# Optimization experiments

Measured on AMD Instinct MI355X. Metric: run time of the kernel, lower is better.

## Reference

```python
import jax, jax.numpy as jnp
import numpy as np

N_FFT = 1024
HOP = 256
WIN_LENGTH = 1024
B = 16
T = 480000


def setup_inputs() -> dict:
    key = jax.random.key(0)
    k1, k2 = jax.random.split(key)
    x = jax.random.normal(k1, (B, T), dtype=jnp.float32)
    window = jax.random.uniform(k2, (WIN_LENGTH,), dtype=jnp.float32)
    return {"x": x, "window": window}


def _dft_kernels(window):
    # pad window to n_fft if needed (here win_length == n_fft)
    if WIN_LENGTH < N_FFT:
        pl = (N_FFT - WIN_LENGTH) // 2
        window = jnp.pad(window, (pl, N_FFT - WIN_LENGTH - pl))
    n_freq = N_FFT // 2 + 1
    k = jnp.arange(n_freq, dtype=jnp.float32)[:, None]   # [F,1]
    n = jnp.arange(N_FFT, dtype=jnp.float32)[None, :]    # [1,N]
    basis = (2.0 * np.pi / N_FFT) * k * n                # [F,N]
    cos_k = jnp.cos(basis) * window[None, :]
    sin_k = -jnp.sin(basis) * window[None, :]
    return cos_k, sin_k


def reference(x, window):
    pad = N_FFT // 2
    xp = jnp.pad(x, ((0, 0), (pad, pad)), mode="reflect")  # center=True, reflect
    n_frames = (xp.shape[1] - N_FFT) // HOP + 1
    # frame extraction: [n_frames, n_fft] gather indices (strided windows)
    idx = jnp.arange(n_frames)[:, None] * HOP + jnp.arange(N_FFT)[None, :]
    frames = xp[:, idx]                                   # [B, n_frames, n_fft]
    cos_k, sin_k = _dft_kernels(window)                   # [F, n_fft]
    real = jnp.einsum("btn,fn->btf", frames, cos_k)        # [B, n_frames, F]
    imag = jnp.einsum("btn,fn->btf", frames, sin_k)
    return jnp.stack([real, imag], axis=-1)               # [B, n_frames, F, 2]
```

## Files before the change

### kernel.cpp

```cpp
#include <hip/hip_runtime.h>

#define BATCH     16
#define T_LEN     480000
#define PAD       512
#define TPAD      481024
#define HOP       256
#define NFRAMES   1876
#define NOUTROW   1026
#define KTOT      1024
#define BCOLS     1152
#define XPSTRIDE  493568

#define BM        256
#define BN        256
#define BK        32
#define NTILES    32
#define TILEA     16384
#define BUFBYTES  32768
#define NBUF      3
#define LDSBYTES  (NBUF * BUFBYTES)

typedef __attribute__((ext_vector_type(8))) short short8;
typedef __attribute__((ext_vector_type(4))) float floatx4;

#define GPTR(p) (const __attribute__((address_space(1))) void*)(p)
#define LPTR(p) (__attribute__((address_space(3))) void*)(p)

__device__ __forceinline__ unsigned short f2bf(float f) {
  union { float f; unsigned int u; } v; v.f = f;
  unsigned int u = v.u;
  return (unsigned short)((u + 0x7FFFu + ((u >> 16) & 1u)) >> 16);
}

__global__ __launch_bounds__(256) void build_xp(const float* __restrict__ x,
                                                unsigned short* __restrict__ xp) {
  const int i0 = (blockIdx.x * 256 + threadIdx.x) * 8;
  const int b  = blockIdx.y;
  const float* xb = x + (size_t)b * T_LEN;
  const int j0 = i0 - PAD;
  union { short8 v; unsigned short u[8]; } o;
  if (j0 >= 0 && j0 + 8 <= T_LEN) {
    const float4 lo = *(const float4*)(xb + j0);
    const float4 hi = *(const float4*)(xb + j0 + 4);
    o.u[0] = f2bf(lo.x); o.u[1] = f2bf(lo.y); o.u[2] = f2bf(lo.z); o.u[3] = f2bf(lo.w);
    o.u[4] = f2bf(hi.x); o.u[5] = f2bf(hi.y); o.u[6] = f2bf(hi.z); o.u[7] = f2bf(hi.w);
  } else {
#pragma unroll
    for (int e = 0; e < 8; ++e) {
      const int i = i0 + e;
      unsigned short v = 0;
      if (i < TPAD) {
        int j = i - PAD;
        if (j < 0) j = -j;
        if (j >= T_LEN) j = 2 * T_LEN - 2 - j;
        v = f2bf(xb[j]);
      }
      o.u[e] = v;
    }
  }
  *(short8*)(xp + (size_t)b * XPSTRIDE + i0) = o.v;
}

__global__ __launch_bounds__(256) void build_bmat(const float* __restrict__ win,
                                                  unsigned short* __restrict__ bm) {
  const int id = blockIdx.x * 256 + threadIdx.x;
  const int j  = id >> 7;
  const int k0 = (id & 127) * 8;
  union { short8 v; unsigned short u[8]; } o;
  if (j < NOUTROW) {
    const int f = j >> 1;
    const float4 w0 = *(const float4*)(win + k0);
    const float4 w1 = *(const float4*)(win + k0 + 4);
    const float wv[8] = {w0.x, w0.y, w0.z, w0.w, w1.x, w1.y, w1.z, w1.w};
#pragma unroll
    for (int e = 0; e < 8; ++e) {
      const int r = (f * (k0 + e)) & (KTOT - 1);
      const float ang = (float)r * 6.1359231515e-3f;
      const float c = __cosf(ang), s = __sinf(ang);
      o.u[e] = f2bf(((j & 1) ? -s : c) * wv[e]);
    }
  } else {
#pragma unroll
    for (int e = 0; e < 8; ++e) o.u[e] = 0;
  }
  *(short8*)(bm + (size_t)j * KTOT + k0) = o.v;
}

__global__ __launch_bounds__(512, 2) void stft_gemm(const unsigned short* __restrict__ xp,
                                                    const unsigned short* __restrict__ bmat,
                                                    float* __restrict__ out) {
  extern __shared__ char smemc[];

  const int tid  = threadIdx.x;
  const int lane = tid & 63;
  const int wv   = tid >> 6;
  const int wm   = wv >> 2;
  const int wn   = wv & 3;
  const int L    = lane & 15;
  const int quad = lane >> 4;
  const int b    = blockIdx.x >> 3;
  const int t0   = (blockIdx.x & 7) * BM;
  const int j0   = blockIdx.y * BN;

  const int srow = tid & 255;
  const int skq  = tid >> 8;
  const unsigned short* asrc =
      xp + (size_t)b * XPSTRIDE + (size_t)(t0 + srow) * HOP + skq * 8;
  int jc = j0 + srow;
  if (jc > BCOLS - 1) jc = BCOLS - 1;
  const unsigned short* bsrc = bmat + (size_t)jc * KTOT + skq * 8;

#define STAGE_A(KT, S)                                                         \
  __builtin_amdgcn_global_load_lds(GPTR(asrc + (KT) * BK),                     \
      LPTR(smemc + (S) * BUFBYTES + tid * 16), 16, 0, 0);                      \
  __builtin_amdgcn_global_load_lds(GPTR(asrc + (KT) * BK + 16),                \
      LPTR(smemc + (S) * BUFBYTES + 8192 + tid * 16), 16, 0, 0)
#define STAGE_B(KT, S)                                                         \
  __builtin_amdgcn_global_load_lds(GPTR(bsrc + (KT) * BK),                     \
      LPTR(smemc + (S) * BUFBYTES + TILEA + tid * 16), 16, 0, 0);              \
  __builtin_amdgcn_global_load_lds(GPTR(bsrc + (KT) * BK + 16),                \
      LPTR(smemc + (S) * BUFBYTES + TILEA + 8192 + tid * 16), 16, 0, 0)

  const int aoff = (quad * 256 + wm * 128 + L) * 16;
  const int boff = TILEA + (quad * 256 + wn * 64 + L) * 16;

  floatx4 acc[8][4] = {};
  short8 af[4], bf[4];

#define PHASE0(C, S, KT2, DOSTAGE)                                             \
  {                                                                            \
    const char* tb_ = smemc + (C) * BUFBYTES;                                  \
    _Pragma("unroll") for (int m = 0; m < 4; ++m)                              \
      af[m] = *(const short8*)(tb_ + aoff + m * 256);                          \
    _Pragma("unroll") for (int n = 0; n < 4; ++n)                              \
      bf[n] = *(const short8*)(tb_ + boff + n * 256);                          \
    if (DOSTAGE) { STAGE_A(KT2, S); }                                          \
    __builtin_amdgcn_s_barrier();                                              \
    __builtin_amdgcn_s_setprio(1);                                             \
    _Pragma("unroll") for (int m = 0; m < 4; ++m)                              \
      _Pragma("unroll") for (int n = 0; n < 4; ++n)                            \
        acc[m][n] = __builtin_amdgcn_mfma_f32_16x16x32_bf16(                   \
            af[m], bf[n], acc[m][n], 0, 0, 0);                                 \
    __builtin_amdgcn_s_setprio(0);                                             \
    __builtin_amdgcn_s_barrier();                                              \
  }
#define PHASE1(C, S, KT2, DOSTAGE, VM)                                         \
  {                                                                            \
    const char* tb_ = smemc + (C) * BUFBYTES;                                  \
    _Pragma("unroll") for (int m = 0; m < 4; ++m)                              \
      af[m] = *(const short8*)(tb_ + aoff + (m + 4) * 256);                    \
    if (DOSTAGE) { STAGE_B(KT2, S); }                                          \
    __builtin_amdgcn_s_barrier();                                              \
    __builtin_amdgcn_s_setprio(1);                                             \
    _Pragma("unroll") for (int m = 0; m < 4; ++m)                              \
      _Pragma("unroll") for (int n = 0; n < 4; ++n)                            \
        acc[m + 4][n] = __builtin_amdgcn_mfma_f32_16x16x32_bf16(               \
            af[m], bf[n], acc[m + 4][n], 0, 0, 0);                             \
    __builtin_amdgcn_s_setprio(0);                                             \
    asm volatile("s_waitcnt vmcnt(" #VM ")" ::: "memory");                     \
    __builtin_amdgcn_s_barrier();                                              \
  }

  STAGE_A(0, 0); STAGE_B(0, 0);
  STAGE_A(1, 1); STAGE_B(1, 1);
  asm volatile("s_waitcnt vmcnt(4)" ::: "memory");
  __builtin_amdgcn_s_barrier();

  for (int g = 0; g < 10; ++g) {
    const int k = 3 * g;
    PHASE0(0, 2, k + 2, 1);  PHASE1(0, 2, k + 2, 1, 4);
    PHASE0(1, 0, k + 3, 1);  PHASE1(1, 0, k + 3, 1, 4);
    PHASE0(2, 1, k + 4, 1);  PHASE1(2, 1, k + 4, 1, 4);
  }
  PHASE0(0, 0, 0, 0);  PHASE1(0, 0, 0, 0, 0);
  PHASE0(1, 0, 0, 0);  PHASE1(1, 0, 0, 0, 0);

#pragma unroll
  for (int mi = 0; mi < 8; ++mi) {
    const int tb = t0 + wm * 128 + mi * 16 + quad * 4;
#pragma unroll
    for (int ni = 0; ni < 4; ++ni) {
      const int gj = j0 + wn * 64 + ni * 16 + L;
      if (gj < NOUTROW) {
#pragma unroll
        for (int i = 0; i < 4; ++i) {
          const int t = tb + i;
          if (t < NFRAMES)
            out[(size_t)(b * NFRAMES + t) * NOUTROW + gj] = acc[mi][ni][i];
        }
      }
    }
  }
}

extern "C" void kernel_launch(void* const* d_in, const int* in_sizes, int n_in,
                              void* d_out, int out_size, void* d_ws, size_t ws_size,
                              hipStream_t stream) {
  const float* x   = (const float*)d_in[0];
  const float* win = (const float*)d_in[1];
  float* out = (float*)d_out;

  unsigned short* xp   = (unsigned short*)d_ws;
  unsigned short* bmat = xp + (size_t)BATCH * XPSTRIDE;

  (void)hipFuncSetAttribute((const void*)stft_gemm,
                            hipFuncAttributeMaxDynamicSharedMemorySize,
                            LDSBYTES);

  build_xp  <<<dim3(XPSTRIDE / 2048, BATCH), 256, 0, stream>>>(x, xp);
  build_bmat<<<dim3(BCOLS * (KTOT / 8) / 256), 256, 0, stream>>>(win, bmat);
  stft_gemm <<<dim3(BATCH * 8, 5), 512, LDSBYTES, stream>>>(xp, bmat, out);
}
```

Before: 259.7 us.

## Split Nyquist bin into separate kernel and shrink GEMM N-tile to avoid padding

The GEMM now covers only the first 1024 output columns (512 frequencies times real and imaginary) with 128-wide N tiles, 256 threads and static double-buffered LDS, replacing the 3-buffer phase-interleaved pipeline. The Nyquist bin (f=512) is computed by a new reduction kernel that writes the last two columns. This removes the padded 1152-column work, of which 126 columns were wasted, but adds an extra launch and uses a simpler, possibly less latency-hiding pipeline. Grid becomes 128x8 blocks.

```diff
diff --git a/kernel.cpp b/kernel.cpp
--- a/kernel.cpp
+++ b/kernel.cpp
@@ -8,17 +8,16 @@
 #define NFRAMES   1876
 #define NOUTROW   1026
 #define KTOT      1024
-#define BCOLS     1152
+#define BCOLS     1024
 #define XPSTRIDE  493568
 
 #define BM        256
-#define BN        256
+#define BN        128
 #define BK        32
 #define NTILES    32
-#define TILEA     16384
-#define BUFBYTES  32768
-#define NBUF      3
-#define LDSBYTES  (NBUF * BUFBYTES)
+#define ABUF      16384
+#define BBUF      8192
+#define BUFB      (ABUF + BBUF)
 
 typedef __attribute__((ext_vector_type(8))) short short8;
 typedef __attribute__((ext_vector_type(4))) float floatx4;
@@ -66,128 +65,128 @@
   const int id = blockIdx.x * 256 + threadIdx.x;
   const int j  = id >> 7;
   const int k0 = (id & 127) * 8;
+  const int f  = j >> 1;
+  const float4 w0 = *(const float4*)(win + k0);
+  const float4 w1 = *(const float4*)(win + k0 + 4);
+  const float wv[8] = {w0.x, w0.y, w0.z, w0.w, w1.x, w1.y, w1.z, w1.w};
   union { short8 v; unsigned short u[8]; } o;
-  if (j < NOUTROW) {
-    const int f = j >> 1;
-    const float4 w0 = *(const float4*)(win + k0);
-    const float4 w1 = *(const float4*)(win + k0 + 4);
-    const float wv[8] = {w0.x, w0.y, w0.z, w0.w, w1.x, w1.y, w1.z, w1.w};
-#pragma unroll
-    for (int e = 0; e < 8; ++e) {
-      const int r = (f * (k0 + e)) & (KTOT - 1);
-      const float ang = (float)r * 6.1359231515e-3f;
-      const float c = __cosf(ang), s = __sinf(ang);
-      o.u[e] = f2bf(((j & 1) ? -s : c) * wv[e]);
-    }
-  } else {
-#pragma unroll
-    for (int e = 0; e < 8; ++e) o.u[e] = 0;
+#pragma unroll
+  for (int e = 0; e < 8; ++e) {
+    const int r = (f * (k0 + e)) & (KTOT - 1);
+    const float ang = (float)r * 6.1359231515e-3f;
+    const float c = __cosf(ang), s = __sinf(ang);
+    o.u[e] = f2bf(((j & 1) ? -s : c) * wv[e]);
   }
   *(short8*)(bm + (size_t)j * KTOT + k0) = o.v;
 }
 
-__global__ __launch_bounds__(512, 2) void stft_gemm(const unsigned short* __restrict__ xp,
+__global__ __launch_bounds__(256) void f512_col(const unsigned short* __restrict__ xp,
+                                                const float* __restrict__ win,
+                                                float* __restrict__ out) {
+  const int t = blockIdx.x * 4 + (threadIdx.x >> 6);
+  const int b = blockIdx.y;
+  const int l = threadIdx.x & 63;
+  const unsigned short* xw = xp + (size_t)b * XPSTRIDE + (size_t)t * HOP;
+  float s = 0.f;
+#pragma unroll
+  for (int j = 0; j < 16; ++j) {
+    const int k = j * 64 + l;
+    union { unsigned int u; float f; } cv;
+    cv.u = (unsigned int)xw[k] << 16;
+    s += win[k] * cv.f;
+  }
+  if (l & 1) s = -s;
+#pragma unroll
+  for (int off = 32; off > 0; off >>= 1) s += __shfl_down(s, off, 64);
+  if (l == 0)
+    *(float2*)(out + (size_t)(b * NFRAMES + t) * NOUTROW + 1024) = make_float2(s, 0.f);
+}
+
+__global__ __launch_bounds__(256, 2) void stft_gemm(const unsigned short* __restrict__ xp,
                                                     const unsigned short* __restrict__ bmat,
                                                     float* __restrict__ out) {
-  extern __shared__ char smemc[];
+  __shared__ char smem[2 * BUFB];
 
   const int tid  = threadIdx.x;
   const int lane = tid & 63;
   const int wv   = tid >> 6;
-  const int wm   = wv >> 2;
-  const int wn   = wv & 3;
+  const int wm   = wv >> 1;
+  const int wn   = wv & 1;
   const int L    = lane & 15;
   const int quad = lane >> 4;
   const int b    = blockIdx.x >> 3;
   const int t0   = (blockIdx.x & 7) * BM;
   const int j0   = blockIdx.y * BN;
 
-  const int srow = tid & 255;
-  const int skq  = tid >> 8;
-  const unsigned short* asrc =
-      xp + (size_t)b * XPSTRIDE + (size_t)(t0 + srow) * HOP + skq * 8;
-  int jc = j0 + srow;
-  if (jc > BCOLS - 1) jc = BCOLS - 1;
-  const unsigned short* bsrc = bmat + (size_t)jc * KTOT + skq * 8;
-
-#define STAGE_A(KT, S)                                                         \
-  __builtin_amdgcn_global_load_lds(GPTR(asrc + (KT) * BK),                     \
-      LPTR(smemc + (S) * BUFBYTES + tid * 16), 16, 0, 0);                      \
-  __builtin_amdgcn_global_load_lds(GPTR(asrc + (KT) * BK + 16),                \
-      LPTR(smemc + (S) * BUFBYTES + 8192 + tid * 16), 16, 0, 0)
-#define STAGE_B(KT, S)                                                         \
-  __builtin_amdgcn_global_load_lds(GPTR(bsrc + (KT) * BK),                     \
-      LPTR(smemc + (S) * BUFBYTES + TILEA + tid * 16), 16, 0, 0);              \
-  __builtin_amdgcn_global_load_lds(GPTR(bsrc + (KT) * BK + 16),                \
-      LPTR(smemc + (S) * BUFBYTES + TILEA + 8192 + tid * 16), 16, 0, 0)
-
-  const int aoff = (quad * 256 + wm * 128 + L) * 16;
-  const int boff = TILEA + (quad * 256 + wn * 64 + L) * 16;
+  const unsigned short* asrc = xp + (size_t)b * XPSTRIDE + (size_t)(t0 + tid) * HOP;
+  const int col = tid & 127;
+  const int kqb = tid >> 7;
+  const unsigned short* bsrc0 = bmat + (size_t)(j0 + col) * KTOT + kqb * 8;
+  const unsigned short* bsrc1 = bmat + (size_t)(j0 + col) * KTOT + (2 + kqb) * 8;
+
+#define STAGE(T1, NB)                                                          \
+  {                                                                            \
+    const int ko_ = (T1) * BK;                                                 \
+    _Pragma("unroll") for (int p = 0; p < 4; ++p)                              \
+      __builtin_amdgcn_global_load_lds(GPTR(asrc + ko_ + p * 8),               \
+          LPTR((NB) + (p * 256 + tid) * 16), 16, 0, 0);                        \
+    __builtin_amdgcn_global_load_lds(GPTR(bsrc0 + ko_),                        \
+        LPTR((NB) + ABUF + tid * 16), 16, 0, 0);                               \
+    __builtin_amdgcn_global_load_lds(GPTR(bsrc1 + ko_),                        \
+        LPTR((NB) + ABUF + (256 + tid) * 16), 16, 0, 0);                       \
+  }
+
+  const int aof = (quad * 256 + wm * 128 + L) * 16;
+  const int bof = ABUF + (quad * 128 + wn * 64 + L) * 16;
 
   floatx4 acc[8][4] = {};
-  short8 af[4], bf[4];
-
-#define PHASE0(C, S, KT2, DOSTAGE)                                             \
-  {                                                                            \
-    const char* tb_ = smemc + (C) * BUFBYTES;                                  \
-    _Pragma("unroll") for (int m = 0; m < 4; ++m)                              \
-      af[m] = *(const short8*)(tb_ + aoff + m * 256);                          \
-    _Pragma("unroll") for (int n = 0; n < 4; ++n)                              \
-      bf[n] = *(const short8*)(tb_ + boff + n * 256);                          \
-    if (DOSTAGE) { STAGE_A(KT2, S); }                                          \
-    __builtin_amdgcn_s_barrier();                                              \
-    __builtin_amdgcn_s_setprio(1);                                             \
-    _Pragma("unroll") for (int m = 0; m < 4; ++m)                              \
-      _Pragma("unroll") for (int n = 0; n < 4; ++n)                            \
-        acc[m][n] = __builtin_amdgcn_mfma_f32_16x16x32_bf16(                   \
-            af[m], bf[n], acc[m][n], 0, 0, 0);                                 \
-    __builtin_amdgcn_s_setprio(0);                                             \
-    __builtin_amdgcn_s_barrier();                                              \
-  }
-#define PHASE1(C, S, KT2, DOSTAGE, VM)                                         \
-  {                                                                            \
-    const char* tb_ = smemc + (C) * BUFBYTES;                                  \
-    _Pragma("unroll") for (int m = 0; m < 4; ++m)                              \
-      af[m] = *(const short8*)(tb_ + aoff + (m + 4) * 256);                    \
-    if (DOSTAGE) { STAGE_B(KT2, S); }                                          \
-    __builtin_amdgcn_s_barrier();                                              \
-    __builtin_amdgcn_s_setprio(1);                                             \
-    _Pragma("unroll") for (int m = 0; m < 4; ++m)                              \
-      _Pragma("unroll") for (int n = 0; n < 4; ++n)                            \
-        acc[m + 4][n] = __builtin_amdgcn_mfma_f32_16x16x32_bf16(               \
-            af[m], bf[n], acc[m + 4][n], 0, 0, 0);                             \
-    __builtin_amdgcn_s_setprio(0);                                             \
-    asm volatile("s_waitcnt vmcnt(" #VM ")" ::: "memory");                     \
-    __builtin_amdgcn_s_barrier();                                              \
-  }
-
-  STAGE_A(0, 0); STAGE_B(0, 0);
-  STAGE_A(1, 1); STAGE_B(1, 1);
-  asm volatile("s_waitcnt vmcnt(4)" ::: "memory");
-  __builtin_amdgcn_s_barrier();
-
-  for (int g = 0; g < 10; ++g) {
-    const int k = 3 * g;
-    PHASE0(0, 2, k + 2, 1);  PHASE1(0, 2, k + 2, 1, 4);
-    PHASE0(1, 0, k + 3, 1);  PHASE1(1, 0, k + 3, 1, 4);
-    PHASE0(2, 1, k + 4, 1);  PHASE1(2, 1, k + 4, 1, 4);
-  }
-  PHASE0(0, 0, 0, 0);  PHASE1(0, 0, 0, 0, 0);
-  PHASE0(1, 0, 0, 0);  PHASE1(1, 0, 0, 0, 0);
-
-#pragma unroll
-  for (int mi = 0; mi < 8; ++mi) {
-    const int tb = t0 + wm * 128 + mi * 16 + quad * 4;
-#pragma unroll
-    for (int ni = 0; ni < 4; ++ni) {
-      const int gj = j0 + wn * 64 + ni * 16 + L;
-      if (gj < NOUTROW) {
-#pragma unroll
-        for (int i = 0; i < 4; ++i) {
-          const int t = tb + i;
-          if (t < NFRAMES)
-            out[(size_t)(b * NFRAMES + t) * NOUTROW + gj] = acc[mi][ni][i];
-        }
+
+  STAGE(0, (char*)smem);
+  __syncthreads();
+
+  for (int T = 0; T < NTILES; ++T) {
+    const char* cb = (const char*)smem + (T & 1) * BUFB;
+    char* nb = (char*)smem + ((T + 1) & 1) * BUFB;
+    if (T + 1 < NTILES) STAGE(T + 1, nb);
+
+    short8 af[4], bf[4];
+#pragma unroll
+    for (int n = 0; n < 4; ++n) bf[n] = *(const short8*)(cb + bof + n * 256);
+#pragma unroll
+    for (int m = 0; m < 4; ++m) af[m] = *(const short8*)(cb + aof + m * 256);
+    __builtin_amdgcn_s_setprio(1);
+#pragma unroll
+    for (int m = 0; m < 4; ++m)
+#pragma unroll
+      for (int n = 0; n < 4; ++n)
+        acc[m][n] = __builtin_amdgcn_mfma_f32_16x16x32_bf16(
+            af[m], bf[n], acc[m][n], 0, 0, 0);
+    __builtin_amdgcn_s_setprio(0);
+#pragma unroll
+    for (int m = 0; m < 4; ++m) af[m] = *(const short8*)(cb + aof + (m + 4) * 256);
+    __builtin_amdgcn_s_setprio(1);
+#pragma unroll
+    for (int m = 0; m < 4; ++m)
+#pragma unroll
+      for (int n = 0; n < 4; ++n)
+        acc[m + 4][n] = __builtin_amdgcn_mfma_f32_16x16x32_bf16(
+            af[m], bf[n], acc[m + 4][n], 0, 0, 0);
+    __builtin_amdgcn_s_setprio(0);
+
+    __syncthreads();
+  }
+
+#pragma unroll
+  for (int mf = 0; mf < 8; ++mf) {
+    const int tb = t0 + wm * 128 + mf * 16 + quad * 4;
+#pragma unroll
+    for (int n = 0; n < 4; ++n) {
+      const int gj = j0 + wn * 64 + n * 16 + L;
+#pragma unroll
+      for (int i = 0; i < 4; ++i) {
+        const int t = tb + i;
+        if (t < NFRAMES)
+          out[(size_t)(b * NFRAMES + t) * NOUTROW + gj] = acc[mf][n][i];
       }
     }
   }
@@ -203,11 +202,8 @@
   unsigned short* xp   = (unsigned short*)d_ws;
   unsigned short* bmat = xp + (size_t)BATCH * XPSTRIDE;
 
-  (void)hipFuncSetAttribute((const void*)stft_gemm,
-                            hipFuncAttributeMaxDynamicSharedMemorySize,
-                            LDSBYTES);
-
   build_xp  <<<dim3(XPSTRIDE / 2048, BATCH), 256, 0, stream>>>(x, xp);
   build_bmat<<<dim3(BCOLS * (KTOT / 8) / 256), 256, 0, stream>>>(win, bmat);
-  stft_gemm <<<dim3(BATCH * 8, 5), 512, LDSBYTES, stream>>>(xp, bmat, out);
-}
+  stft_gemm <<<dim3(BATCH * 8, BCOLS / BN), 256, 0, stream>>>(xp, bmat, out);
+  f512_col  <<<dim3(NFRAMES / 4, BATCH), 256, 0, stream>>>(xp, win, out);
+}
```

Result: slower. 272.3 us (+4.9%).
